# Kernel tuning notes

Hardware: AMD Instinct MI355X
Metric: run time of the kernel (lower is better)

## Reference

```python
import jax, jax.numpy as jnp
import numpy as np

N_NODES = 100000
N_EDGES = 1600000
IN_F, HID_F, OUT_F = 64, 64, 16


def setup_inputs() -> dict:
    key = jax.random.key(0)
    k_x, k_e, k_w1, k_w2 = jax.random.split(key, 4)
    x = jax.random.normal(k_x, (N_NODES, IN_F), dtype=jnp.float32)
    edge_index = jax.random.randint(k_e, (2, N_EDGES), 0, N_NODES, dtype=jnp.int64)
    # Glorot-ish init for the GCNConv linear weights; bias zeros (PyG default)
    W1 = jax.random.normal(k_w1, (IN_F, HID_F), dtype=jnp.float32) / np.sqrt(IN_F)
    b1 = jnp.zeros((HID_F,), dtype=jnp.float32)
    W2 = jax.random.normal(k_w2, (HID_F, OUT_F), dtype=jnp.float32) / np.sqrt(HID_F)
    b2 = jnp.zeros((OUT_F,), dtype=jnp.float32)
    return {"x": x, "edge_index": edge_index, "W1": W1, "b1": b1, "W2": W2, "b2": b2}


def reference(x, edge_index, W1, b1, W2, b2):
    N = x.shape[0]
    # GCNConv: add self-loops, symmetric normalization D^-1/2 A D^-1/2
    loop = jnp.arange(N, dtype=edge_index.dtype)
    src = jnp.concatenate([edge_index[0], loop])  # [E+N]
    dst = jnp.concatenate([edge_index[1], loop])  # [E+N]
    deg = jax.ops.segment_sum(jnp.ones_like(dst, dtype=x.dtype), dst, num_segments=N)
    dis = jax.lax.rsqrt(deg)  # deg >= 1 due to self-loops
    norm = dis[src] * dis[dst]  # [E+N]

    def gcn_conv(h, W, b):
        h = h @ W                                   # [N, d_out]
        msg = h[src] * norm[:, None]                # gather + scale  [E+N, d_out]
        agg = jax.ops.segment_sum(msg, dst, num_segments=N)  # scatter-add
        return agg + b

    h = jax.nn.relu(gcn_conv(x, W1, b1))
    h = gcn_conv(h, W2, b2)
    return jax.nn.log_softmax(h, axis=1)
```

## Files before the change

kernel.cpp:

```cpp
#include <hip/hip_runtime.h>
#include <hip/hip_bf16.h>
#include <hip/hip_fp16.h>


#define F1 64
#define F2 16
#define NBKT 256
#define BSH 512
#define NSB 256
#define SBD 512
#define STG 9216

typedef _Float16 f16x8 __attribute__((ext_vector_type(8)));
typedef _Float16 f16x4 __attribute__((ext_vector_type(4)));
typedef float f32x4 __attribute__((ext_vector_type(4)));

__device__ inline f16x8 shfl_xor_f16x8(f16x8 v, int off) {
  union U { f16x8 h; int i[4]; } a, b;
  a.h = v;
#pragma unroll
  for (int k = 0; k < 4; ++k) b.i[k] = __shfl_xor(a.i[k], off);
  return b.h;
}
__device__ inline f16x4 shfl_xor_f16x4(f16x4 v, int off) {
  union U { f16x4 h; int i[2]; } a, b;
  a.h = v;
#pragma unroll
  for (int k = 0; k < 2; ++k) b.i[k] = __shfl_xor(a.i[k], off);
  return b.h;
}

__global__ void k_scatterL(const int* __restrict__ src, const int* __restrict__ dst,
                           int* __restrict__ tmp, int* __restrict__ segstart,
                           int* __restrict__ bcnt, int E, int nb, int chunk) {
  __shared__ int h[NBKT];
  __shared__ int cur[NBKT];
  __shared__ int sc[NBKT];
  int t = threadIdx.x, sb = blockIdx.x;
  int beg = sb * chunk, end = min(beg + chunk, E);
  for (int i = t; i < NBKT; i += SBD) h[i] = 0;
  __syncthreads();
  int e;
  for (e = beg + t * 4; e + 4 <= end; e += 4 * SBD) {
    int4 d4 = *(const int4*)(dst + e);
    atomicAdd(&h[d4.x >> 9], 1);
    atomicAdd(&h[d4.y >> 9], 1);
    atomicAdd(&h[d4.z >> 9], 1);
    atomicAdd(&h[d4.w >> 9], 1);
  }
  for (; e < end; ++e) atomicAdd(&h[dst[e] >> 9], 1);
  __syncthreads();
  for (int i = t; i < nb; i += SBD)
    if (h[i]) atomicAdd(&bcnt[i], h[i]);
  if (t < NBKT) sc[t] = h[t];
  __syncthreads();
  for (int off = 1; off < NBKT; off <<= 1) {
    int a = (t < NBKT && t >= off) ? sc[t - off] : 0;
    __syncthreads();
    if (t < NBKT) sc[t] += a;
    __syncthreads();
  }
  if (t < NBKT) cur[t] = (t == 0) ? 0 : sc[t - 1];
  __syncthreads();
  for (int i = t; i < nb; i += SBD) segstart[sb * (nb + 1) + i] = beg + cur[i];
  if (t == 0) segstart[sb * (nb + 1) + nb] = end;
  __syncthreads();
  for (e = beg + t * 4; e + 4 <= end; e += 4 * SBD) {
    int4 d4 = *(const int4*)(dst + e);
    int4 s4 = *(const int4*)(src + e);
    int b, off;
    b = d4.x >> 9; off = atomicAdd(&cur[b], 1); tmp[beg + off] = (s4.x << 9) | (d4.x & 511);
    b = d4.y >> 9; off = atomicAdd(&cur[b], 1); tmp[beg + off] = (s4.y << 9) | (d4.y & 511);
    b = d4.z >> 9; off = atomicAdd(&cur[b], 1); tmp[beg + off] = (s4.z << 9) | (d4.z & 511);
    b = d4.w >> 9; off = atomicAdd(&cur[b], 1); tmp[beg + off] = (s4.w << 9) | (d4.w & 511);
  }
  for (; e < end; ++e) {
    int d = dst[e];
    int b = d >> 9;
    int off = atomicAdd(&cur[b], 1);
    tmp[beg + off] = (src[e] << 9) | (d & 511);
  }
}

__global__ void k_misc(const int* __restrict__ bcnt, int* __restrict__ bbase, int nb,
                       const float* __restrict__ W1, const float* __restrict__ W2,
                       __half* __restrict__ W1T, __half* __restrict__ W2T) {
  int t = threadIdx.x;
  if (blockIdx.x == 0) {
    __shared__ int lds[1024];
    lds[t] = (t < nb) ? bcnt[t] : 0;
    __syncthreads();
    for (int off = 1; off < 1024; off <<= 1) {
      int add = (t >= off) ? lds[t - off] : 0;
      __syncthreads();
      lds[t] += add;
      __syncthreads();
    }
    if (t < nb) bbase[t] = (t == 0) ? 0 : lds[t - 1];
  } else {
    for (int i = t; i < 64 * 64; i += 1024) {
      int n = i >> 6, k = i & 63;
      W1T[i] = __float2half(W1[k * 64 + n]);
    }
    for (int i = t; i < 16 * 64; i += 1024) {
      int n = i >> 6, k = i & 63;
      W2T[i] = __float2half(W2[k * 16 + n]);
    }
  }
}

__global__ void k_csr(const int* __restrict__ tmp, const int* __restrict__ segstart,
                      const int* __restrict__ bbase, int* __restrict__ csr,
                      int* __restrict__ rowptr, float* __restrict__ dis,
                      int N, int nb) {
  __shared__ int stage[STG];
  __shared__ int sc[BSH];
  __shared__ int cnt[BSH];
  __shared__ int lofs[BSH];
  int b = blockIdx.x, t = threadIdx.x;
  int s0 = 0, len = 0;
  if (t < NSB) {
    s0 = segstart[t * (nb + 1) + b];
    len = segstart[t * (nb + 1) + b + 1] - s0;
  }
  if (t < NSB) sc[t] = len;
  __syncthreads();
  for (int off = 1; off < NSB; off <<= 1) {
    int a = (t < NSB && t >= off) ? sc[t - off] : 0;
    __syncthreads();
    if (t < NSB) sc[t] += a;
    __syncthreads();
  }
  int total = sc[NSB - 1];
  int my0 = (t == 0) ? 0 : ((t < NSB) ? sc[t - 1] : 0);
  if (t < NSB) {
    int i = 0;
    for (; i + 4 <= len; i += 4) {
      int v0 = tmp[s0 + i], v1 = tmp[s0 + i + 1], v2 = tmp[s0 + i + 2], v3 = tmp[s0 + i + 3];
      stage[my0 + i] = v0; stage[my0 + i + 1] = v1;
      stage[my0 + i + 2] = v2; stage[my0 + i + 3] = v3;
    }
    for (; i < len; ++i) stage[my0 + i] = tmp[s0 + i];
  }
  cnt[t] = 0;
  __syncthreads();
  for (int i = t; i < total; i += BSH) atomicAdd(&cnt[stage[i] & (BSH - 1)], 1);
  __syncthreads();
  sc[t] = cnt[t];
  __syncthreads();
  for (int off = 1; off < BSH; off <<= 1) {
    int a = (t >= off) ? sc[t - off] : 0;
    __syncthreads();
    sc[t] += a;
    __syncthreads();
  }
  int beg = bbase[b];
  int excl = (t == 0) ? 0 : sc[t - 1];
  lofs[t] = excl;
  int n = b * BSH + t;
  if (n <= N) rowptr[n] = beg + excl;
  if (n < N) dis[n] = rsqrtf((float)(cnt[t] + 1));
  cnt[t] = 0;
  __syncthreads();
  for (int i = t; i < total; i += BSH) {
    int p = stage[i];
    int l = p & (BSH - 1);
    int off = atomicAdd(&cnt[l], 1);
    csr[beg + lofs[l] + off] = p >> 9;
  }
}

__global__ void k_gemm1(const float* __restrict__ x, const __half* __restrict__ W1T,
                        const float* __restrict__ dis, __half* __restrict__ out, int N) {
  int t = threadIdx.x;
  int wv = t >> 6, lane = t & 63;
  int m = lane & 15, q = lane >> 4;
  int row0 = blockIdx.x * 64 + wv * 16;
  int arow = min(row0 + m, N - 1);
  const _Float16* wt = (const _Float16*)W1T;
  f16x8 bf[4][2];
#pragma unroll
  for (int c = 0; c < 4; ++c)
#pragma unroll
    for (int kt = 0; kt < 2; ++kt)
      bf[c][kt] = *(const f16x8*)&wt[(c * 16 + m) * 64 + kt * 32 + q * 8];
  f16x8 a[2];
#pragma unroll
  for (int kt = 0; kt < 2; ++kt) {
    const float4* xp = (const float4*)(x + (size_t)arow * 64 + kt * 32 + q * 8);
    float4 u = xp[0], v = xp[1];
    a[kt][0] = (_Float16)u.x; a[kt][1] = (_Float16)u.y;
    a[kt][2] = (_Float16)u.z; a[kt][3] = (_Float16)u.w;
    a[kt][4] = (_Float16)v.x; a[kt][5] = (_Float16)v.y;
    a[kt][6] = (_Float16)v.z; a[kt][7] = (_Float16)v.w;
  }
  f32x4 acc[4] = {};
#pragma unroll
  for (int kt = 0; kt < 2; ++kt)
#pragma unroll
    for (int c = 0; c < 4; ++c)
      acc[c] = __builtin_amdgcn_mfma_f32_16x16x32_f16(a[kt], bf[c][kt], acc[c], 0, 0, 0);
#pragma unroll
  for (int r = 0; r < 4; ++r) {
    int n = row0 + q * 4 + r;
    if (n < N) {
      float dn = dis[n];
#pragma unroll
      for (int c = 0; c < 4; ++c)
        out[(size_t)n * 64 + c * 16 + m] = __float2half(acc[c][r] * dn);
    }
  }
}

__global__ void k_agg1f(const __half* __restrict__ h, const float* __restrict__ dis,
                        const int* __restrict__ rowptr, const int* __restrict__ csr,
                        const float* __restrict__ b1, const __half* __restrict__ W2T,
                        __half* __restrict__ h2, int N) {
  int gt = blockIdx.x * blockDim.x + threadIdx.x;
  int n = gt >> 6;
  if (n >= N) return;
  int lane = gt & 63;
  int fl = lane & 7;
  int sub = lane >> 3;
  const _Float16* hp = (const _Float16*)h;
  float dn = dis[n];
  float4 bu = *(const float4*)(b1 + fl * 8);
  float4 bv = *(const float4*)(b1 + fl * 8 + 4);
  const _Float16* wt = (const _Float16*)W2T;
  f16x8 w0 = *(const f16x8*)&wt[(sub * 2 + 0) * 64 + fl * 8];
  f16x8 w1 = *(const f16x8*)&wt[(sub * 2 + 1) * 64 + fl * 8];
  f16x8 acc0 = {}, acc1 = {};
  if (sub == 0)
    acc0 = *(const f16x8*)&hp[(size_t)n * 64 + fl * 8];
  int beg = rowptr[n], end = rowptr[n + 1];
  int e = beg + sub;
  int sA = (e < end) ? csr[e] : -1;
  int sB = (e + 8 < end) ? csr[e + 8] : -1;
  while (sB >= 0) {
    int e2 = e + 16;
    int sC = (e2 < end) ? csr[e2] : -1;
    int sD = (e2 + 8 < end) ? csr[e2 + 8] : -1;
    f16x8 v0 = *(const f16x8*)&hp[(size_t)sA * 64 + fl * 8];
    f16x8 v1 = *(const f16x8*)&hp[(size_t)sB * 64 + fl * 8];
    acc0 += v0;
    acc1 += v1;
    sA = sC; sB = sD; e = e2;
  }
  if (sA >= 0)
    acc0 += *(const f16x8*)&hp[(size_t)sA * 64 + fl * 8];
  f16x8 acc = acc0 + acc1;
  acc += shfl_xor_f16x8(acc, 8);
  acc += shfl_xor_f16x8(acc, 16);
  acc += shfl_xor_f16x8(acc, 32);
  float bb[8] = {bu.x, bu.y, bu.z, bu.w, bv.x, bv.y, bv.z, bv.w};
  float hrow[8];
#pragma unroll
  for (int k = 0; k < 8; ++k)
    hrow[k] = fmaxf(fmaf(dn, (float)acc[k], bb[k]), 0.f);
  float p0 = 0.f, p1 = 0.f;
#pragma unroll
  for (int k = 0; k < 8; ++k) {
    p0 = fmaf(hrow[k], (float)w0[k], p0);
    p1 = fmaf(hrow[k], (float)w1[k], p1);
  }
  p0 += __shfl_xor(p0, 1); p1 += __shfl_xor(p1, 1);
  p0 += __shfl_xor(p0, 2); p1 += __shfl_xor(p1, 2);
  p0 += __shfl_xor(p0, 4); p1 += __shfl_xor(p1, 4);
  if (fl == 0) {
    __half2 o;
    o.x = __float2half(p0 * dn);
    o.y = __float2half(p1 * dn);
    *(__half2*)((_Float16*)h2 + (size_t)n * 16 + sub * 2) = o;
  }
}

__global__ void k_agg2(const __half* __restrict__ h2, const float* __restrict__ dis,
                       const int* __restrict__ rowptr, const int* __restrict__ csr,
                       const float* __restrict__ b2, float* __restrict__ out, int N) {
  int gt = blockIdx.x * blockDim.x + threadIdx.x;
  int n = gt >> 6;
  if (n >= N) return;
  int lane = gt & 63;
  int fl = lane & 3;
  int sub = lane >> 2;
  const _Float16* hp = (const _Float16*)h2;
  f16x4 acc0 = {}, acc1 = {};
  if (sub == 0)
    acc0 = *(const f16x4*)&hp[(size_t)n * 16 + fl * 4];
  int beg = rowptr[n], end = rowptr[n + 1];
  int e = beg + sub;
  int sA = (e < end) ? csr[e] : -1;
  int sB = (e + 16 < end) ? csr[e + 16] : -1;
  while (sB >= 0) {
    int e2 = e + 32;
    int sC = (e2 < end) ? csr[e2] : -1;
    int sD = (e2 + 16 < end) ? csr[e2 + 16] : -1;
    f16x4 v0 = *(const f16x4*)&hp[(size_t)sA * 16 + fl * 4];
    f16x4 v1 = *(const f16x4*)&hp[(size_t)sB * 16 + fl * 4];
    acc0 += v0;
    acc1 += v1;
    sA = sC; sB = sD; e = e2;
  }
  if (sA >= 0)
    acc0 += *(const f16x4*)&hp[(size_t)sA * 16 + fl * 4];
  f16x4 acc = acc0 + acc1;
  acc += shfl_xor_f16x4(acc, 4);
  acc += shfl_xor_f16x4(acc, 8);
  acc += shfl_xor_f16x4(acc, 16);
  acc += shfl_xor_f16x4(acc, 32);
  if (sub == 0) {
    float dn = dis[n];
    float4 bb = *(const float4*)(b2 + fl * 4);
    float v0 = fmaf(dn, (float)acc[0], bb.x);
    float v1 = fmaf(dn, (float)acc[1], bb.y);
    float v2 = fmaf(dn, (float)acc[2], bb.z);
    float v3 = fmaf(dn, (float)acc[3], bb.w);
    float m = fmaxf(fmaxf(v0, v1), fmaxf(v2, v3));
    m = fmaxf(m, __shfl_xor(m, 1));
    m = fmaxf(m, __shfl_xor(m, 2));
    float s2 = __expf(v0 - m) + __expf(v1 - m) + __expf(v2 - m) + __expf(v3 - m);
    s2 += __shfl_xor(s2, 1);
    s2 += __shfl_xor(s2, 2);
    float ls = m + __logf(s2);
    float4 o = {v0 - ls, v1 - ls, v2 - ls, v3 - ls};
    *(float4*)(out + (size_t)n * 16 + fl * 4) = o;
  }
}

extern "C" void kernel_launch(void* const* d_in, const int* in_sizes, int n_in,
                              void* d_out, int out_size, void* d_ws, size_t ws_size,
                              hipStream_t stream) {
  const float* x = (const float*)d_in[0];
  const int* ei = (const int*)d_in[1];
  const float* W1 = (const float*)d_in[2];
  const float* b1 = (const float*)d_in[3];
  const float* W2 = (const float*)d_in[4];
  const float* b2 = (const float*)d_in[5];
  float* out = (float*)d_out;

  int N = in_sizes[0] / F1;
  int E = in_sizes[1] / 2;
  const int* src = ei;
  const int* dst = ei + E;
  int nb = (N + BSH - 1) >> 9;
  int chunk = ((E + NSB - 1) / NSB + 3) & ~3;

  char* ws = (char*)d_ws;
  size_t o_bcnt  = 0;
  size_t o_bbase = o_bcnt + NBKT * 4;
  size_t o_w1t   = o_bbase + NBKT * 4;
  size_t o_w2t   = o_w1t + 64 * 64 * 2;
  size_t o_seg   = (o_w2t + 16 * 64 * 2 + 255) & ~(size_t)255;
  size_t o_dis   = (o_seg + (size_t)NSB * (nb + 1) * 4 + 255) & ~(size_t)255;
  size_t o_rowp  = (o_dis + (size_t)N * 4 + 255) & ~(size_t)255;
  size_t o_tmp   = (o_rowp + (size_t)(N + 1) * 4 + 255) & ~(size_t)255;
  size_t o_csr   = (o_tmp + (size_t)NSB * chunk * 4 + 255) & ~(size_t)255;
  size_t o_h1    = (o_csr + (size_t)E * 4 + 255) & ~(size_t)255;
  size_t o_h2    = (o_h1 + (size_t)N * 64 * 2 + 255) & ~(size_t)255;

  int* bcnt    = (int*)(ws + o_bcnt);
  int* bbase   = (int*)(ws + o_bbase);
  __half* W1T  = (__half*)(ws + o_w1t);
  __half* W2T  = (__half*)(ws + o_w2t);
  int* segst   = (int*)(ws + o_seg);
  float* dis   = (float*)(ws + o_dis);
  int* rowptr  = (int*)(ws + o_rowp);
  int* tmp     = (int*)(ws + o_tmp);
  int* csr     = (int*)(ws + o_csr);
  __half* h1   = (__half*)(ws + o_h1);
  __half* h2   = (__half*)(ws + o_h2);

  hipMemsetAsync(bcnt, 0, NBKT * 4, stream);

  k_scatterL<<<NSB, SBD, 0, stream>>>(src, dst, tmp, segst, bcnt, E, nb, chunk);
  k_misc<<<2, 1024, 0, stream>>>(bcnt, bbase, nb, W1, W2, W1T, W2T);
  k_csr<<<nb, BSH, 0, stream>>>(tmp, segst, bbase, csr, rowptr, dis, N, nb);

  int gb = (N + 63) / 64;
  k_gemm1<<<gb, 256, 0, stream>>>(x, W1T, dis, h1, N);
  k_agg1f<<<((size_t)N * 64 + 255) / 256, 256, 0, stream>>>(h1, dis, rowptr, csr, b1, W2T, h2, N);
  k_agg2<<<((size_t)N * 64 + 255) / 256, 256, 0, stream>>>(h2, dis, rowptr, csr, b2, out, N);
}
```

Baseline: 203.6 us.

## Remove k_misc launch, fold bucket prefix into k_csr, use packed fp16 dot

The separate k_misc kernel is eliminated. The weight transpose now runs in an extra block of k_scatterL, and each k_csr block computes its own exclusive prefix over the bucket counts. This removes one kernel launch and its serialization point, at the cost of every k_csr block running a redundant prefix scan. Independently, the scatter block size is raised from 512 to 1024, and the layer-2 projection dot product in the aggregation kernel switches from fp32 FMAs to packed fp16 multiply-adds, which lowers precision.

```diff
diff --git a/kernel.cpp b/kernel.cpp
--- a/kernel.cpp
+++ b/kernel.cpp
@@ -8,11 +8,12 @@
 #define NBKT 256
 #define BSH 512
 #define NSB 256
-#define SBD 512
+#define SBD 1024
 #define STG 9216
 
 typedef _Float16 f16x8 __attribute__((ext_vector_type(8)));
 typedef _Float16 f16x4 __attribute__((ext_vector_type(4)));
+typedef _Float16 f16x2 __attribute__((ext_vector_type(2)));
 typedef float f32x4 __attribute__((ext_vector_type(4)));
 
 __device__ inline f16x8 shfl_xor_f16x8(f16x8 v, int off) {
@@ -32,11 +33,24 @@
 
 __global__ void k_scatterL(const int* __restrict__ src, const int* __restrict__ dst,
                            int* __restrict__ tmp, int* __restrict__ segstart,
-                           int* __restrict__ bcnt, int E, int nb, int chunk) {
+                           int* __restrict__ bcnt, int E, int nb, int chunk,
+                           const float* __restrict__ W1, const float* __restrict__ W2,
+                           __half* __restrict__ W1T, __half* __restrict__ W2T) {
+  int t = threadIdx.x, sb = blockIdx.x;
+  if (sb == NSB) {
+    for (int i = t; i < 64 * 64; i += SBD) {
+      int n = i >> 6, k = i & 63;
+      W1T[i] = __float2half(W1[k * 64 + n]);
+    }
+    for (int i = t; i < 16 * 64; i += SBD) {
+      int n = i >> 6, k = i & 63;
+      W2T[i] = __float2half(W2[k * 16 + n]);
+    }
+    return;
+  }
   __shared__ int h[NBKT];
   __shared__ int cur[NBKT];
   __shared__ int sc[NBKT];
-  int t = threadIdx.x, sb = blockIdx.x;
   int beg = sb * chunk, end = min(beg + chunk, E);
   for (int i = t; i < NBKT; i += SBD) h[i] = 0;
   __syncthreads();
@@ -82,48 +96,33 @@
   }
 }
 
-__global__ void k_misc(const int* __restrict__ bcnt, int* __restrict__ bbase, int nb,
-                       const float* __restrict__ W1, const float* __restrict__ W2,
-                       __half* __restrict__ W1T, __half* __restrict__ W2T) {
-  int t = threadIdx.x;
-  if (blockIdx.x == 0) {
-    __shared__ int lds[1024];
-    lds[t] = (t < nb) ? bcnt[t] : 0;
-    __syncthreads();
-    for (int off = 1; off < 1024; off <<= 1) {
-      int add = (t >= off) ? lds[t - off] : 0;
-      __syncthreads();
-      lds[t] += add;
-      __syncthreads();
-    }
-    if (t < nb) bbase[t] = (t == 0) ? 0 : lds[t - 1];
-  } else {
-    for (int i = t; i < 64 * 64; i += 1024) {
-      int n = i >> 6, k = i & 63;
-      W1T[i] = __float2half(W1[k * 64 + n]);
-    }
-    for (int i = t; i < 16 * 64; i += 1024) {
-      int n = i >> 6, k = i & 63;
-      W2T[i] = __float2half(W2[k * 16 + n]);
-    }
-  }
-}
-
 __global__ void k_csr(const int* __restrict__ tmp, const int* __restrict__ segstart,
-                      const int* __restrict__ bbase, int* __restrict__ csr,
+                      const int* __restrict__ bcnt, int* __restrict__ csr,
                       int* __restrict__ rowptr, float* __restrict__ dis,
                       int N, int nb) {
   __shared__ int stage[STG];
   __shared__ int sc[BSH];
   __shared__ int cnt[BSH];
   __shared__ int lofs[BSH];
+  __shared__ int s_beg;
   int b = blockIdx.x, t = threadIdx.x;
+  sc[t] = (t < b) ? bcnt[t] : 0;
+  __syncthreads();
+  for (int off = 1; off < BSH; off <<= 1) {
+    int a = (t >= off) ? sc[t - off] : 0;
+    __syncthreads();
+    sc[t] += a;
+    __syncthreads();
+  }
+  if (t == 0) s_beg = sc[BSH - 1];
+  __syncthreads();
+  int beg = s_beg;
   int s0 = 0, len = 0;
   if (t < NSB) {
     s0 = segstart[t * (nb + 1) + b];
     len = segstart[t * (nb + 1) + b + 1] - s0;
   }
-  if (t < NSB) sc[t] = len;
+  sc[t] = (t < NSB) ? len : 0;
   __syncthreads();
   for (int off = 1; off < NSB; off <<= 1) {
     int a = (t < NSB && t >= off) ? sc[t - off] : 0;
@@ -154,7 +153,6 @@
     sc[t] += a;
     __syncthreads();
   }
-  int beg = bbase[b];
   int excl = (t == 0) ? 0 : sc[t - 1];
   lofs[t] = excl;
   int n = b * BSH + t;
@@ -253,16 +251,21 @@
   acc += shfl_xor_f16x8(acc, 16);
   acc += shfl_xor_f16x8(acc, 32);
   float bb[8] = {bu.x, bu.y, bu.z, bu.w, bv.x, bv.y, bv.z, bv.w};
-  float hrow[8];
+  f16x8 hr16;
 #pragma unroll
   for (int k = 0; k < 8; ++k)
-    hrow[k] = fmaxf(fmaf(dn, (float)acc[k], bb[k]), 0.f);
-  float p0 = 0.f, p1 = 0.f;
-#pragma unroll
-  for (int k = 0; k < 8; ++k) {
-    p0 = fmaf(hrow[k], (float)w0[k], p0);
-    p1 = fmaf(hrow[k], (float)w1[k], p1);
-  }
+    hr16[k] = (_Float16)fmaxf(fmaf(dn, (float)acc[k], bb[k]), 0.f);
+  const f16x2* h2v = (const f16x2*)&hr16;
+  const f16x2* w0v = (const f16x2*)&w0;
+  const f16x2* w1v = (const f16x2*)&w1;
+  f16x2 q0 = {}, q1 = {};
+#pragma unroll
+  for (int k = 0; k < 4; ++k) {
+    q0 += h2v[k] * w0v[k];
+    q1 += h2v[k] * w1v[k];
+  }
+  float p0 = (float)q0[0] + (float)q0[1];
+  float p1 = (float)q1[0] + (float)q1[1];
   p0 += __shfl_xor(p0, 1); p1 += __shfl_xor(p1, 1);
   p0 += __shfl_xor(p0, 2); p1 += __shfl_xor(p1, 2);
   p0 += __shfl_xor(p0, 4); p1 += __shfl_xor(p1, 4);
@@ -347,8 +350,7 @@
 
   char* ws = (char*)d_ws;
   size_t o_bcnt  = 0;
-  size_t o_bbase = o_bcnt + NBKT * 4;
-  size_t o_w1t   = o_bbase + NBKT * 4;
+  size_t o_w1t   = o_bcnt + NBKT * 4;
   size_t o_w2t   = o_w1t + 64 * 64 * 2;
   size_t o_seg   = (o_w2t + 16 * 64 * 2 + 255) & ~(size_t)255;
   size_t o_dis   = (o_seg + (size_t)NSB * (nb + 1) * 4 + 255) & ~(size_t)255;
@@ -359,7 +361,6 @@
   size_t o_h2    = (o_h1 + (size_t)N * 64 * 2 + 255) & ~(size_t)255;
 
   int* bcnt    = (int*)(ws + o_bcnt);
-  int* bbase   = (int*)(ws + o_bbase);
   __half* W1T  = (__half*)(ws + o_w1t);
   __half* W2T  = (__half*)(ws + o_w2t);
   int* segst   = (int*)(ws + o_seg);
@@ -372,9 +373,9 @@
 
   hipMemsetAsync(bcnt, 0, NBKT * 4, stream);
 
-  k_scatterL<<<NSB, SBD, 0, stream>>>(src, dst, tmp, segst, bcnt, E, nb, chunk);
-  k_misc<<<2, 1024, 0, stream>>>(bcnt, bbase, nb, W1, W2, W1T, W2T);
-  k_csr<<<nb, BSH, 0, stream>>>(tmp, segst, bbase, csr, rowptr, dis, N, nb);
+  k_scatterL<<<NSB + 1, SBD, 0, stream>>>(src, dst, tmp, segst, bcnt, E, nb, chunk,
+                                          W1, W2, W1T, W2T);
+  k_csr<<<nb, BSH, 0, stream>>>(tmp, segst, bcnt, csr, rowptr, dis, N, nb);
 
   int gb = (N + 63) / 64;
   k_gemm1<<<gb, 256, 0, stream>>>(x, W1T, dis, h1, N);
```

Measured after the change: 200.7 us. No clear change (-1.4%).
